# Performance work log

Measured on AMD Instinct MI355X. Metric: run time of the kernel, lower is better.

Reference implementation:

```python
import jax, jax.numpy as jnp
import numpy as np

EPS = 1e-7
KERNELS = ((5, 5), (7, 1), (1, 7))
SCALES = (60, 30, 15, 8)


def avg_pool(x, kh, kw):
    # PyTorch AvgPool2d(kernel, stride=1, padding=(kh//2, kw//2)), count_include_pad=True
    s = jax.lax.reduce_window(x, 0.0, jax.lax.add, (1, 1, kh, kw), (1, 1, 1, 1),
                              ((0, 0), (0, 0), (kh // 2, kh // 2), (kw // 2, kw // 2)))
    return s / (kh * kw)


def resize_bilinear(x, oh, ow):
    # F.interpolate(mode='bilinear', align_corners=True), NCHW
    B, C, H, W = x.shape
    def coords(o, s):
        pos = jnp.arange(o) * ((s - 1) / max(o - 1, 1))
        i0 = jnp.floor(pos).astype(jnp.int32)
        i1 = jnp.minimum(i0 + 1, s - 1)
        w = (pos - i0).astype(x.dtype)
        return w, i0, i1
    wy, y0, y1 = coords(oh, H)
    wx, x0, x1 = coords(ow, W)
    rows = x[:, :, y0, :] * (1 - wy)[None, None, :, None] + x[:, :, y1, :] * wy[None, None, :, None]
    return rows[:, :, :, x0] * (1 - wx) + rows[:, :, :, x1] * wx


def setup_inputs() -> dict:
    key = jax.random.key(0)
    ks = jax.random.split(key, 12)
    B, C, H, shot = 2, 1024, 60, 1
    hid, tdim = 256, 300
    return {
        "weight": jax.random.uniform(ks[0], (B, shot, 1, 1), dtype=jnp.float32),
        "query_feat_4": jax.random.normal(ks[1], (B, C, H, H), dtype=jnp.float32),
        "supp_feats": jax.random.normal(ks[2], (shot, B, C, H, H), dtype=jnp.float32),
        "masks": jax.random.uniform(ks[3], (shot, B, 1, 473, 473), dtype=jnp.float32),
        "k": jax.random.normal(ks[4], (B, hid, H, H), dtype=jnp.float32),
        "text": jax.random.normal(ks[5], (B, tdim), dtype=jnp.float32),
        "prototype": jax.random.normal(ks[6], (B, hid, 1, 1), dtype=jnp.float32),
        "w_q": jax.random.normal(ks[7], (tdim + hid, hid), dtype=jnp.float32) * 0.05,
        "w_k": jax.random.normal(ks[8], (hid, hid), dtype=jnp.float32) * 0.05,
        "w_bl": jax.random.normal(ks[9], (hid, hid), dtype=jnp.float32) * 0.05,
        "w_proj": jax.random.normal(ks[10], (hid, hid), dtype=jnp.float32) * 0.05,
        "b_proj": jnp.zeros((hid,), dtype=jnp.float32),
    }


def reference(weight, query_feat_4, supp_feats, masks, k, text, prototype, w_q, w_k, w_bl, w_proj, b_proj):
    # ---------------- SPM: self-activation prior mask ----------------
    B, C, H, W = query_feat_4.shape
    S = H * W
    # pooled query features per kernel (shared across supports)
    q_pooled = []
    for (kh, kw) in KERNELS:
        tq = avg_pool(query_feat_4, kh, kw).reshape(B, C, S)
        tq_t = jnp.transpose(tq, (0, 2, 1))                    # [B,S,C]
        qn = jnp.sqrt((tq_t ** 2).sum(-1, keepdims=True))      # [B,S,1]
        q_pooled.append((tq_t, qn))

    corr_list = []
    for i in range(supp_feats.shape[0]):  # loop over shot (small, fixed)
        tmp_mask = resize_bilinear(masks[i], H, W)
        s = supp_feats[i] * tmp_mask
        region = []
        for (kh, kw), (tq_t, qn) in zip(KERNELS, q_pooled):
            ts = avg_pool(s, kh, kw).reshape(B, C, S)          # [B,C,S]
            sn = jnp.sqrt((ts ** 2).sum(1, keepdims=True))     # [B,1,S]
            sim = jnp.matmul(tq_t, ts) / (jnp.matmul(qn, sn) + EPS) * qn  # [B,S,S]
            sim = sim.mean(2)                                  # [B,S]
            mn = sim.min(1, keepdims=True)
            mx = sim.max(1, keepdims=True)
            sim = (sim - mn) / (mx - mn + EPS)
            region.append(sim.reshape(B, H, W))
        corr_list.append(jnp.stack(region, 1).mean(1))         # [B,H,W]
    corr = jnp.stack(corr_list, 1)                             # [B,shot,H,W]
    corr1 = (weight * corr).sum(1, keepdims=True)              # [B,1,H,W]
    corr2 = resize_bilinear(corr1, SCALES[1], SCALES[1])
    corr3 = resize_bilinear(corr1, SCALES[2], SCALES[2])
    corr4 = resize_bilinear(corr1, SCALES[3], SCALES[3])

    # ---------------- APA: bi-linear cross-modal attention ----------------
    Bk, hid, h, w = k.shape
    proto = prototype.reshape(Bk, 1, hid)                      # [B,1,hid]
    q = jnp.concatenate([text[:, None, :], proto], axis=-1)    # [B,1,embed]
    kx = jnp.einsum('oi,bihw->bohw', w_k, k).reshape(Bk, hid, h * w)
    kx = jnp.transpose(kx, (0, 2, 1))                          # [B,S,hid]
    qx = jnp.einsum('bqe,eh->bqh', q, w_q)                     # [B,1,hid]
    qw = jnp.einsum('bqh,hd->bqd', qx, w_bl)                   # bi_linear score
    score = jnp.einsum('bqd,bsd->bqs', qw, kx)                 # [B,1,S]
    score = jax.nn.softmax(score, axis=-1)
    out = jnp.einsum('bqs,bsd->bqd', score, kx)
    out = jnp.einsum('bqd,do->bqo', out, w_proj) + b_proj      # proj (dropout=eval no-op)
    out = out + proto
    return corr1, corr2, corr3, corr4, out
```

## Files before the change

### kernel.cpp

```cpp
#include <hip/hip_runtime.h>
#include <math.h>

#define EPSF 1e-7f
#define Bsz 2
#define Cch 1024
#define Hh 60
#define Ssz 3600
#define HID 256
#define TDIM 300
#define MH 473

#define TROWS 15
#define LROWS 21
#define LPITCH 68
#define CPG 8

#define OFF_SN2    0
#define OFF_WMAP   21600
#define OFF_V      43200
#define OFF_U      49344
#define OFF_KBAR   49856
#define OFF_DOTP   50368
#define OFF_SCOREP 395968
#define ZERO_WS    21600
#define ZERO_OUT   9578

__global__ void k_zero(float* __restrict__ ws, float* __restrict__ out) {
    int i = blockIdx.x * 256 + threadIdx.x;
    if (i < ZERO_WS) ws[i] = 0.f;
    else if (i < ZERO_WS + ZERO_OUT) out[i - ZERO_WS] = 0.f;
}

__global__ void __launch_bounds__(256) k_pool_sn2(const float* __restrict__ supp,
                                                  const float* __restrict__ masks,
                                                  float* __restrict__ sn2g) {
    __shared__ float  mk[LROWS * LPITCH];
    __shared__ float2 raw[LROWS * LPITCH];
    __shared__ float2 h5s[LROWS * LPITCH];
    __shared__ float2 h7s[LROWS * LPITCH];
    int tid = threadIdx.x;
    int tile = blockIdx.x;
    int cg = blockIdx.y;
    int b = blockIdx.z;
    int y0 = tile * TROWS;

    const float2 z2 = {0.f, 0.f};
    for (int i = tid; i < LROWS * LPITCH; i += 256) {
        mk[i] = 0.f; raw[i] = z2; h5s[i] = z2; h7s[i] = z2;
    }
    __syncthreads();

    int lr[5], lx[5]; bool lv[5], la[5];
    #pragma unroll
    for (int j = 0; j < 5; ++j) {
        int idx = tid + 256 * j;
        int r = idx / 60, x = idx - 60 * r;
        lr[j] = r; lx[j] = x;
        la[j] = idx < 1260;
        int iy = y0 - 3 + r;
        lv[j] = la[j] && (iy >= 0) && (iy < Hh);
    }
    #pragma unroll
    for (int j = 0; j < 5; ++j)
        if (lv[j]) {
            int iy = y0 - 3 + lr[j];
            mk[lr[j] * LPITCH + 4 + lx[j]] =
                masks[(size_t)b * MH * MH + (size_t)(iy * 8) * MH + lx[j] * 8];
        }

    int orow[4], ox[4]; bool ov[4];
    #pragma unroll
    for (int j = 0; j < 4; ++j) {
        int o = tid + 256 * j;
        int oy = o / 60, x = o - 60 * oy;
        orow[j] = oy + 3; ox[j] = x; ov[j] = o < 900;
    }
    float a0[4] = {0,0,0,0}, a1[4] = {0,0,0,0}, a2[4] = {0,0,0,0};

    const float* chbase = supp + ((size_t)b * Cch + (size_t)cg * CPG) * Ssz + (y0 - 3) * 60;
    float pf0[5], pf1[5];
    #pragma unroll
    for (int j = 0; j < 5; ++j) {
        pf0[j] = lv[j] ? chbase[tid + 256 * j] : 0.f;
        pf1[j] = lv[j] ? chbase[Ssz + tid + 256 * j] : 0.f;
    }

    for (int p = 0; p < CPG / 2; ++p) {
        __syncthreads();
        #pragma unroll
        for (int j = 0; j < 5; ++j)
            if (lv[j]) {
                float m = mk[lr[j] * LPITCH + 4 + lx[j]];
                raw[lr[j] * LPITCH + 4 + lx[j]] = make_float2(pf0[j] * m, pf1[j] * m);
            }
        __syncthreads();
        #pragma unroll
        for (int j = 0; j < 5; ++j)
            if (la[j]) {
                int base = lr[j] * LPITCH + 4 + lx[j];
                float2 m3 = raw[base - 3], m2 = raw[base - 2], m1 = raw[base - 1];
                float2 c0 = raw[base], p1 = raw[base + 1], p2 = raw[base + 2], p3 = raw[base + 3];
                float2 h5, h7;
                h5.x = m2.x + m1.x + c0.x + p1.x + p2.x;
                h5.y = m2.y + m1.y + c0.y + p1.y + p2.y;
                h7.x = h5.x + m3.x + p3.x;
                h7.y = h5.y + m3.y + p3.y;
                h5s[base] = h5; h7s[base] = h7;
            }
        __syncthreads();
        if (p + 1 < CPG / 2) {
            const float* nb = chbase + (size_t)(2 * p + 2) * Ssz;
            #pragma unroll
            for (int j = 0; j < 5; ++j) {
                pf0[j] = lv[j] ? nb[tid + 256 * j] : 0.f;
                pf1[j] = lv[j] ? nb[Ssz + tid + 256 * j] : 0.f;
            }
        }
        #pragma unroll
        for (int j = 0; j < 4; ++j)
            if (ov[j]) {
                int base = orow[j] * LPITCH + 4 + ox[j];
                float2 sa = h5s[base - 2*LPITCH], sb = h5s[base - LPITCH], sc0 = h5s[base];
                float2 sd = h5s[base + LPITCH], se = h5s[base + 2*LPITCH];
                float p55x = (sa.x + sb.x + sc0.x + sd.x + se.x) * (1.f / 25.f);
                float p55y = (sa.y + sb.y + sc0.y + sd.y + se.y) * (1.f / 25.f);
                float2 ra = raw[base - 3*LPITCH], rb = raw[base - 2*LPITCH], rc = raw[base - LPITCH];
                float2 rd = raw[base], re = raw[base + LPITCH], rf = raw[base + 2*LPITCH], rg = raw[base + 3*LPITCH];
                float p71x = (ra.x + rb.x + rc.x + rd.x + re.x + rf.x + rg.x) * (1.f / 7.f);
                float p71y = (ra.y + rb.y + rc.y + rd.y + re.y + rf.y + rg.y) * (1.f / 7.f);
                float2 h7v = h7s[base];
                float p17x = h7v.x * (1.f / 7.f), p17y = h7v.y * (1.f / 7.f);
                a0[j] += p55x * p55x + p55y * p55y;
                a1[j] += p71x * p71x + p71y * p71y;
                a2[j] += p17x * p17x + p17y * p17y;
            }
    }
    float* g0 = sn2g + ((size_t)b * 3 + 0) * Ssz;
    float* g1 = sn2g + ((size_t)b * 3 + 1) * Ssz;
    float* g2 = sn2g + ((size_t)b * 3 + 2) * Ssz;
    #pragma unroll
    for (int j = 0; j < 4; ++j)
        if (ov[j]) {
            int q = (y0 + orow[j] - 3) * 60 + ox[j];
            atomicAdd(&g0[q], a0[j]);
            atomicAdd(&g1[q], a1[j]);
            atomicAdd(&g2[q], a2[j]);
        }
}

__global__ void k_wmap(const float* __restrict__ sn2g, const float* __restrict__ masks,
                       float* __restrict__ wmapg) {
    __shared__ float inv[LROWS * LPITCH];
    int tile = blockIdx.x;
    int bk = blockIdx.y;
    int b = bk / 3, kt = bk % 3;
    int tid = threadIdx.x;
    int y0 = tile * TROWS;
    for (int i = tid; i < LROWS * LPITCH; i += 256) inv[i] = 0.f;
    __syncthreads();
    const float* sn2 = sn2g + (size_t)bk * Ssz;
    #pragma unroll
    for (int j = 0; j < 5; ++j) {
        int idx = tid + 256 * j;
        if (idx < 1260) {
            int r = idx / 60, x = idx - 60 * r;
            int iy = y0 - 3 + r;
            if (iy >= 0 && iy < Hh)
                inv[r * LPITCH + 4 + x] = 1.0f / sqrtf(fmaxf(sn2[iy * 60 + x], 1e-30f));
        }
    }
    __syncthreads();
    int kh = (kt == 0) ? 5 : (kt == 1) ? 7 : 1;
    int kw = (kt == 0) ? 5 : (kt == 2) ? 7 : 1;
    int rh = kh / 2, rw = kw / 2;
    float norm = 1.f / (float)(kh * kw);
    #pragma unroll
    for (int j = 0; j < 4; ++j) {
        int o = tid + 256 * j;
        if (o < 900) {
            int oy = o / 60, x = o - 60 * oy;
            int base = (oy + 3) * LPITCH + 4 + x;
            float s = 0.f;
            for (int dy = -rh; dy <= rh; ++dy)
                for (int dx = -rw; dx <= rw; ++dx)
                    s += inv[base + dy * LPITCH + dx];
            int gy = y0 + oy;
            float m = masks[(size_t)b * MH * MH + (size_t)(gy * 8) * MH + x * 8];
            wmapg[(size_t)bk * Ssz + gy * 60 + x] = s * norm * m;
        }
    }
}

__global__ void k_v(const float* __restrict__ supp, float* __restrict__ ws) {
    int c = blockIdx.x, b = blockIdx.y;
    int tid = threadIdx.x;
    int lane = tid & 63, w = tid >> 6;
    const float4* sp4 = (const float4*)(supp + ((size_t)b * Cch + c) * Ssz);
    const float4* w04 = (const float4*)(ws + OFF_WMAP + (size_t)(b * 3 + 0) * Ssz);
    const float4* w14 = (const float4*)(ws + OFF_WMAP + (size_t)(b * 3 + 1) * Ssz);
    const float4* w24 = (const float4*)(ws + OFF_WMAP + (size_t)(b * 3 + 2) * Ssz);
    float a0 = 0, a1 = 0, a2 = 0;
    #pragma unroll
    for (int j = 0; j < 4; ++j) {
        int idx = tid + 256 * j;
        if (idx < 900) {
            float4 f = sp4[idx];
            float4 g0 = w04[idx], g1 = w14[idx], g2 = w24[idx];
            a0 += f.x * g0.x + f.y * g0.y + f.z * g0.z + f.w * g0.w;
            a1 += f.x * g1.x + f.y * g1.y + f.z * g1.z + f.w * g1.w;
            a2 += f.x * g2.x + f.y * g2.y + f.z * g2.z + f.w * g2.w;
        }
    }
    #pragma unroll
    for (int m = 32; m >= 1; m >>= 1) {
        a0 += __shfl_xor(a0, m, 64);
        a1 += __shfl_xor(a1, m, 64);
        a2 += __shfl_xor(a2, m, 64);
    }
    __shared__ float r[3][4];
    if (lane == 0) { r[0][w] = a0; r[1][w] = a1; r[2][w] = a2; }
    __syncthreads();
    if (tid < 3) {
        float s = r[tid][0] + r[tid][1] + r[tid][2] + r[tid][3];
        ws[OFF_V + (size_t)(b * 3 + tid) * Cch + c] = s;
    }
}

__global__ void k_dot(const float* __restrict__ query, float* __restrict__ ws) {
    int qt = blockIdx.x, cc = blockIdx.y, b = blockIdx.z;
    int q = qt * 256 + threadIdx.x;
    if (q >= Ssz) return;
    const float* v0 = ws + OFF_V + (size_t)(b * 3 + 0) * Cch;
    const float* v1 = ws + OFF_V + (size_t)(b * 3 + 1) * Cch;
    const float* v2 = ws + OFF_V + (size_t)(b * 3 + 2) * Cch;
    float a0 = 0, a1 = 0, a2 = 0;
    int c0 = cc * 64;
    #pragma unroll 8
    for (int c = c0; c < c0 + 64; ++c) {
        float qv = query[((size_t)b * Cch + c) * Ssz + q];
        a0 += qv * v0[c]; a1 += qv * v1[c]; a2 += qv * v2[c];
    }
    float* dst = ws + OFF_DOTP + (size_t)((cc * 2 + b) * 3) * Ssz + q;
    dst[0] = a0; dst[Ssz] = a1; dst[2 * Ssz] = a2;
}

__global__ void __launch_bounds__(1024) k_sim(const float* __restrict__ weight,
                                              float* __restrict__ ws,
                                              float* __restrict__ out) {
    __shared__ float dpad[66 * LPITCH];
    __shared__ float hbuf[66 * LPITCH];
    __shared__ float rmin[16], rmax[16];
    int bk = blockIdx.x; int b = bk / 3; int kt = bk % 3;
    int tid = threadIdx.x;
    int lane = tid & 63, w = tid >> 6;

    const float* dp0 = ws + OFF_DOTP + (size_t)(b * 3 + kt) * Ssz;
    for (int i = tid; i < 66 * LPITCH; i += 1024) {
        int r = i / LPITCH, col = i - r * LPITCH;
        int y = r - 3, x = col - 4;
        float s = 0.f;
        if (y >= 0 && y < Hh && x >= 0 && x < Hh) {
            int q = y * Hh + x;
            #pragma unroll
            for (int g = 0; g < 16; ++g) s += dp0[(size_t)g * 6 * Ssz + q];
        }
        dpad[i] = s;
    }
    __syncthreads();
    if (kt != 1) {
        for (int idx = tid; idx < 66 * 60; idx += 1024) {
            int r = idx / 60, x = idx - 60 * r;
            int base = r * LPITCH + 4 + x;
            if (kt == 0) {
                hbuf[base] = dpad[base - 2] + dpad[base - 1] + dpad[base]
                           + dpad[base + 1] + dpad[base + 2];
            } else {
                hbuf[base] = dpad[base - 3] + dpad[base - 2] + dpad[base - 1] + dpad[base]
                           + dpad[base + 1] + dpad[base + 2] + dpad[base + 3];
            }
        }
    }
    __syncthreads();
    float norm = ((kt == 0) ? (1.f / 25.f) : (1.f / 7.f)) * (1.f / (float)Ssz);
    float vals[4];
    float vmin = INFINITY, vmax = -INFINITY;
    #pragma unroll
    for (int j = 0; j < 4; ++j) {
        int q = tid + j * 1024;
        if (q < Ssz) {
            int y = q / Hh, x = q - y * Hh;
            int base = (y + 3) * LPITCH + 4 + x;
            float s;
            if (kt == 0)
                s = hbuf[base - 2*LPITCH] + hbuf[base - LPITCH] + hbuf[base]
                  + hbuf[base + LPITCH] + hbuf[base + 2*LPITCH];
            else if (kt == 1)
                s = dpad[base - 3*LPITCH] + dpad[base - 2*LPITCH] + dpad[base - LPITCH]
                  + dpad[base] + dpad[base + LPITCH] + dpad[base + 2*LPITCH] + dpad[base + 3*LPITCH];
            else
                s = hbuf[base];
            float val = s * norm;
            vals[j] = val;
            vmin = fminf(vmin, val); vmax = fmaxf(vmax, val);
        }
    }
    #pragma unroll
    for (int m = 32; m >= 1; m >>= 1) {
        vmin = fminf(vmin, __shfl_xor(vmin, m, 64));
        vmax = fmaxf(vmax, __shfl_xor(vmax, m, 64));
    }
    if (lane == 0) { rmin[w] = vmin; rmax[w] = vmax; }
    __syncthreads();
    float mn = rmin[0], mx = rmax[0];
    #pragma unroll
    for (int ww = 1; ww < 16; ++ww) {
        mn = fminf(mn, rmin[ww]); mx = fmaxf(mx, rmax[ww]);
    }
    float inv = 1.f / (mx - mn + EPSF);
    float wq3 = weight[b] * (1.f / 3.f);
    __syncthreads();
    #pragma unroll
    for (int j = 0; j < 4; ++j) {
        int q = tid + j * 1024;
        if (q < Ssz) {
            float vn = (vals[j] - mn) * inv;
            atomicAdd(&out[b * Ssz + q], wq3 * vn);
            hbuf[q] = vn;
        }
    }
    __syncthreads();
    #pragma unroll
    for (int j = 0; j < 2; ++j) {
        int o = tid + j * 1024;
        if (o >= 1189) continue;
        int O, p, outi;
        if (o < 900)       { O = 30; p = o;        outi = 7200 + b * 900 + p; }
        else if (o < 1125) { O = 15; p = o - 900;  outi = 9000 + b * 225 + p; }
        else               { O = 8;  p = o - 1125; outi = 9450 + b * 64 + p; }
        int y = p / O, x = p - y * O;
        float sc = 59.f / (float)(O - 1);
        float py = y * sc, px = x * sc;
        int y0 = (int)floorf(py), x0 = (int)floorf(px);
        int y1 = min(y0 + 1, 59), x1 = min(x0 + 1, 59);
        float wy = py - y0, wx = px - x0;
        float v = hbuf[y0 * 60 + x0] * (1.f - wy) * (1.f - wx)
                + hbuf[y1 * 60 + x0] * wy * (1.f - wx)
                + hbuf[y0 * 60 + x1] * (1.f - wy) * wx
                + hbuf[y1 * 60 + x1] * wy * wx;
        atomicAdd(&out[outi], wq3 * v);
    }
}

__global__ void __launch_bounds__(1024, 1)
k_apa_u(const float* __restrict__ text, const float* __restrict__ proto,
        const float* __restrict__ w_q, const float* __restrict__ w_bl,
        const float* __restrict__ w_k, float* __restrict__ ws) {
    int b = blockIdx.x;
    int tid = threadIdx.x;
    int lane = tid & 63, w = tid >> 6;
    __shared__ float4 p4[16][64];
    __shared__ float qxs[256], qws[256];
    const float4* wq4 = (const float4*)w_q;
    const float4* wbl4 = (const float4*)w_bl;
    const float4* wk4 = (const float4*)w_k;

    float4 acc = {0.f, 0.f, 0.f, 0.f};
    #pragma unroll
    for (int j = 0; j < 35; ++j) {
        int e = w + 16 * j;
        if (e < TDIM + HID) {
            float x = (e < TDIM) ? text[b * TDIM + e] : proto[b * HID + e - TDIM];
            float4 f = wq4[(size_t)e * 64 + lane];
            acc.x += x * f.x; acc.y += x * f.y; acc.z += x * f.z; acc.w += x * f.w;
        }
    }
    p4[w][lane] = acc;
    __syncthreads();
    if (tid < 256) {
        const float* pf = (const float*)p4;
        float s = 0.f;
        #pragma unroll
        for (int ww = 0; ww < 16; ++ww) s += pf[ww * 256 + tid];
        qxs[tid] = s;
    }
    __syncthreads();

    acc.x = acc.y = acc.z = acc.w = 0.f;
    #pragma unroll
    for (int j = 0; j < 16; ++j) {
        int e = w + 16 * j;
        float x = qxs[e];
        float4 f = wbl4[(size_t)e * 64 + lane];
        acc.x += x * f.x; acc.y += x * f.y; acc.z += x * f.z; acc.w += x * f.w;
    }
    p4[w][lane] = acc;
    __syncthreads();
    if (tid < 256) {
        const float* pf = (const float*)p4;
        float s = 0.f;
        #pragma unroll
        for (int ww = 0; ww < 16; ++ww) s += pf[ww * 256 + tid];
        qws[tid] = s;
    }
    __syncthreads();

    acc.x = acc.y = acc.z = acc.w = 0.f;
    #pragma unroll
    for (int j = 0; j < 16; ++j) {
        int e = w + 16 * j;
        float x = qws[e];
        float4 f = wk4[(size_t)e * 64 + lane];
        acc.x += x * f.x; acc.y += x * f.y; acc.z += x * f.z; acc.w += x * f.w;
    }
    p4[w][lane] = acc;
    __syncthreads();
    if (tid < 256) {
        const float* pf = (const float*)p4;
        float s = 0.f;
        #pragma unroll
        for (int ww = 0; ww < 16; ++ww) s += pf[ww * 256 + tid];
        ws[OFF_U + b * HID + tid] = s;
    }
}

__global__ void k_score(const float* __restrict__ kin, float* __restrict__ ws) {
    int st = blockIdx.x, g = blockIdx.y, b = blockIdx.z;
    int s = st * 256 + threadIdx.x;
    if (s >= Ssz) return;
    const float* u = ws + OFF_U + b * HID;
    float acc = 0.f;
    int i0 = g * 64;
    #pragma unroll 8
    for (int i = i0; i < i0 + 64; ++i)
        acc += u[i] * kin[((size_t)b * HID + i) * Ssz + s];
    ws[OFF_SCOREP + (size_t)(g * 2 + b) * Ssz + s] = acc;
}

__global__ void k_kbar(const float* __restrict__ kin, float* __restrict__ ws) {
    int i = blockIdx.x, b = blockIdx.y;
    int tid = threadIdx.x;
    int lane = tid & 63, w = tid >> 6;
    __shared__ float r1[4], r2[4];
    const float4* s0 = (const float4*)(ws + OFF_SCOREP + (size_t)(0 * 2 + b) * Ssz);
    const float4* s1 = (const float4*)(ws + OFF_SCOREP + (size_t)(1 * 2 + b) * Ssz);
    const float4* s2 = (const float4*)(ws + OFF_SCOREP + (size_t)(2 * 2 + b) * Ssz);
    const float4* s3 = (const float4*)(ws + OFF_SCOREP + (size_t)(3 * 2 + b) * Ssz);
    float4 sv[4]; bool act[4];
    float mx = -INFINITY;
    #pragma unroll
    for (int j = 0; j < 4; ++j) {
        int idx = tid + 256 * j;
        act[j] = idx < 900;
        if (act[j]) {
            float4 a = s0[idx], c = s1[idx], d = s2[idx], e = s3[idx];
            float4 v;
            v.x = a.x + c.x + d.x + e.x;
            v.y = a.y + c.y + d.y + e.y;
            v.z = a.z + c.z + d.z + e.z;
            v.w = a.w + c.w + d.w + e.w;
            sv[j] = v;
            mx = fmaxf(mx, fmaxf(fmaxf(v.x, v.y), fmaxf(v.z, v.w)));
        }
    }
    #pragma unroll
    for (int m = 32; m >= 1; m >>= 1) mx = fmaxf(mx, __shfl_xor(mx, m, 64));
    if (lane == 0) r1[w] = mx;
    __syncthreads();
    mx = fmaxf(fmaxf(r1[0], r1[1]), fmaxf(r1[2], r1[3]));
    __syncthreads();
    const float4* kr = (const float4*)(kin + ((size_t)b * HID + i) * Ssz);
    float se = 0.f, wsum = 0.f;
    #pragma unroll
    for (int j = 0; j < 4; ++j) {
        if (act[j]) {
            int idx = tid + 256 * j;
            float4 v = sv[j];
            float ex = expf(v.x - mx), ey = expf(v.y - mx);
            float ez = expf(v.z - mx), ew = expf(v.w - mx);
            se += ex + ey + ez + ew;
            float4 k4 = kr[idx];
            wsum += ex * k4.x + ey * k4.y + ez * k4.z + ew * k4.w;
        }
    }
    #pragma unroll
    for (int m = 32; m >= 1; m >>= 1) {
        se += __shfl_xor(se, m, 64);
        wsum += __shfl_xor(wsum, m, 64);
    }
    if (lane == 0) { r1[w] = se; r2[w] = wsum; }
    __syncthreads();
    if (tid == 0) {
        float seT = r1[0] + r1[1] + r1[2] + r1[3];
        float wsT = r2[0] + r2[1] + r2[2] + r2[3];
        ws[OFF_KBAR + b * HID + i] = wsT / seT;
    }
}

__global__ void __launch_bounds__(1024, 1)
k_apa_out(const float* __restrict__ w_k, const float* __restrict__ w_proj,
          const float* __restrict__ b_proj, const float* __restrict__ proto,
          const float* __restrict__ ws, float* __restrict__ out) {
    int b = blockIdx.x;
    int tid = threadIdx.x;
    int lane = tid & 63, w = tid >> 6;
    __shared__ float4 kbs[64];
    __shared__ float o1s[256];
    __shared__ float4 p4[16][64];
    const float4* wk4 = (const float4*)w_k;
    const float4* wp4 = (const float4*)w_proj;

    if (tid < 64) kbs[tid] = ((const float4*)(ws + OFF_KBAR + b * HID))[tid];
    __syncthreads();

    float4 kb4 = kbs[lane];
    #pragma unroll
    for (int r = 0; r < 16; ++r) {
        int h = w + 16 * r;
        float4 f = wk4[(size_t)h * 64 + lane];
        float p = f.x * kb4.x + f.y * kb4.y + f.z * kb4.z + f.w * kb4.w;
        #pragma unroll
        for (int m = 32; m >= 1; m >>= 1) p += __shfl_xor(p, m, 64);
        if (lane == 0) o1s[h] = p;
    }
    __syncthreads();

    float4 acc = {0.f, 0.f, 0.f, 0.f};
    #pragma unroll
    for (int j = 0; j < 16; ++j) {
        int d = w + 16 * j;
        float x = o1s[d];
        float4 f = wp4[(size_t)d * 64 + lane];
        acc.x += x * f.x; acc.y += x * f.y; acc.z += x * f.z; acc.w += x * f.w;
    }
    p4[w][lane] = acc;
    __syncthreads();
    if (tid < 256) {
        const float* pf = (const float*)p4;
        float s = 0.f;
        #pragma unroll
        for (int ww = 0; ww < 16; ++ww) s += pf[ww * 256 + tid];
        out[9578 + b * HID + tid] = s + b_proj[tid] + proto[b * HID + tid];
    }
}

extern "C" void kernel_launch(void* const* d_in, const int* in_sizes, int n_in,
                              void* d_out, int out_size, void* d_ws, size_t ws_size,
                              hipStream_t stream) {
    const float* weight = (const float*)d_in[0];
    const float* query  = (const float*)d_in[1];
    const float* supp   = (const float*)d_in[2];
    const float* masks  = (const float*)d_in[3];
    const float* kin    = (const float*)d_in[4];
    const float* text   = (const float*)d_in[5];
    const float* proto  = (const float*)d_in[6];
    const float* w_q    = (const float*)d_in[7];
    const float* w_k    = (const float*)d_in[8];
    const float* w_bl   = (const float*)d_in[9];
    const float* w_proj = (const float*)d_in[10];
    const float* b_proj = (const float*)d_in[11];
    float* out = (float*)d_out;
    float* ws  = (float*)d_ws;

    k_zero<<<(ZERO_WS + ZERO_OUT + 255) / 256, 256, 0, stream>>>(ws, out);

    k_pool_sn2<<<dim3(4, Cch / CPG, Bsz), 256, 0, stream>>>(supp, masks, ws + OFF_SN2);
    k_wmap<<<dim3(4, 6), 256, 0, stream>>>(ws + OFF_SN2, masks, ws + OFF_WMAP);
    k_v<<<dim3(Cch, Bsz), 256, 0, stream>>>(supp, ws);
    k_dot<<<dim3(15, 16, Bsz), 256, 0, stream>>>(query, ws);
    k_sim<<<6, 1024, 0, stream>>>(weight, ws, out);

    k_apa_u<<<Bsz, 1024, 0, stream>>>(text, proto, w_q, w_bl, w_k, ws);
    k_score<<<dim3(15, 4, Bsz), 256, 0, stream>>>(kin, ws);
    k_kbar<<<dim3(HID, Bsz), 256, 0, stream>>>(kin, ws);
    k_apa_out<<<Bsz, 1024, 0, stream>>>(w_k, w_proj, b_proj, proto, ws, out);
}
```

Before: 209.5 us.

## Merge kernel chain with in-kernel spin flags, drop atomics and zeroing pass

```diff
diff --git a/kernel.cpp b/kernel.cpp
--- a/kernel.cpp
+++ b/kernel.cpp
@@ -15,25 +15,28 @@
 #define LPITCH 68
 #define CPG 8
 
-#define OFF_SN2    0
-#define OFF_WMAP   21600
-#define OFF_V      43200
-#define OFF_U      49344
-#define OFF_KBAR   49856
-#define OFF_DOTP   50368
-#define OFF_SCOREP 395968
-#define ZERO_WS    21600
-#define ZERO_OUT   9578
-
-__global__ void k_zero(float* __restrict__ ws, float* __restrict__ out) {
-    int i = blockIdx.x * 256 + threadIdx.x;
-    if (i < ZERO_WS) ws[i] = 0.f;
-    else if (i < ZERO_WS + ZERO_OUT) out[i - ZERO_WS] = 0.f;
+#define OFF_PPOOL  0
+#define OFF_WMAP   2764800
+#define OFF_V      2786400
+#define OFF_DOTP   2792544
+#define OFF_NORM   3138144
+#define OFF_SCORE  3159744
+#define OFF_KBAR   3166944
+#define OFF_CNT    3167456
+
+__device__ __forceinline__ void spin_until(int* p, int target) {
+    while (__hip_atomic_load(p, __ATOMIC_ACQUIRE, __HIP_MEMORY_SCOPE_AGENT) < target)
+        __builtin_amdgcn_s_sleep(10);
+}
+__device__ __forceinline__ void publish(int* p, int tid) {
+    __threadfence();
+    __syncthreads();
+    if (tid == 0) __hip_atomic_fetch_add(p, 1, __ATOMIC_RELEASE, __HIP_MEMORY_SCOPE_AGENT);
 }
 
 __global__ void __launch_bounds__(256) k_pool_sn2(const float* __restrict__ supp,
                                                   const float* __restrict__ masks,
-                                                  float* __restrict__ sn2g) {
+                                                  float* __restrict__ ws) {
     __shared__ float  mk[LROWS * LPITCH];
     __shared__ float2 raw[LROWS * LPITCH];
     __shared__ float2 h5s[LROWS * LPITCH];
@@ -135,21 +138,16 @@
                 a2[j] += p17x * p17x + p17y * p17y;
             }
     }
-    float* g0 = sn2g + ((size_t)b * 3 + 0) * Ssz;
-    float* g1 = sn2g + ((size_t)b * 3 + 1) * Ssz;
-    float* g2 = sn2g + ((size_t)b * 3 + 2) * Ssz;
+    float* dst = ws + OFF_PPOOL + (size_t)(cg * 2 + b) * 3 * Ssz;
     #pragma unroll
     for (int j = 0; j < 4; ++j)
         if (ov[j]) {
             int q = (y0 + orow[j] - 3) * 60 + ox[j];
-            atomicAdd(&g0[q], a0[j]);
-            atomicAdd(&g1[q], a1[j]);
-            atomicAdd(&g2[q], a2[j]);
-        }
-}
-
-__global__ void k_wmap(const float* __restrict__ sn2g, const float* __restrict__ masks,
-                       float* __restrict__ wmapg) {
+            dst[q] = a0[j]; dst[Ssz + q] = a1[j]; dst[2 * Ssz + q] = a2[j];
+        }
+}
+
+__global__ void k_wmap(const float* __restrict__ masks, float* __restrict__ ws) {
     __shared__ float inv[LROWS * LPITCH];
     int tile = blockIdx.x;
     int bk = blockIdx.y;
@@ -158,15 +156,20 @@
     int y0 = tile * TROWS;
     for (int i = tid; i < LROWS * LPITCH; i += 256) inv[i] = 0.f;
     __syncthreads();
-    const float* sn2 = sn2g + (size_t)bk * Ssz;
+    const float* pp = ws + OFF_PPOOL + (size_t)(b * 3 + kt) * Ssz;
     #pragma unroll
     for (int j = 0; j < 5; ++j) {
         int idx = tid + 256 * j;
         if (idx < 1260) {
             int r = idx / 60, x = idx - 60 * r;
             int iy = y0 - 3 + r;
-            if (iy >= 0 && iy < Hh)
-                inv[r * LPITCH + 4 + x] = 1.0f / sqrtf(fmaxf(sn2[iy * 60 + x], 1e-30f));
+            if (iy >= 0 && iy < Hh) {
+                int q = iy * 60 + x;
+                float s = 0.f;
+                #pragma unroll 4
+                for (int g = 0; g < 128; ++g) s += pp[(size_t)g * (6 * Ssz) + q];
+                inv[r * LPITCH + 4 + x] = 1.0f / sqrtf(fmaxf(s, 1e-30f));
+            }
         }
     }
     __syncthreads();
@@ -186,180 +189,210 @@
                     s += inv[base + dy * LPITCH + dx];
             int gy = y0 + oy;
             float m = masks[(size_t)b * MH * MH + (size_t)(gy * 8) * MH + x * 8];
-            wmapg[(size_t)bk * Ssz + gy * 60 + x] = s * norm * m;
+            ws[OFF_WMAP + (size_t)bk * Ssz + gy * 60 + x] = s * norm * m;
         }
     }
 }
 
 __global__ void k_v(const float* __restrict__ supp, float* __restrict__ ws) {
-    int c = blockIdx.x, b = blockIdx.y;
-    int tid = threadIdx.x;
-    int lane = tid & 63, w = tid >> 6;
-    const float4* sp4 = (const float4*)(supp + ((size_t)b * Cch + c) * Ssz);
+    int cB = blockIdx.x, b = blockIdx.y;
+    int tid = threadIdx.x, lane = tid & 63, w = tid >> 6;
+    if (cB == 0 && b == 0 && tid < 3) ((int*)(ws + OFF_CNT))[tid] = 0;
+    int c0 = cB * 4;
+    const float4* sp4 = (const float4*)(supp + ((size_t)b * Cch + c0) * Ssz);
     const float4* w04 = (const float4*)(ws + OFF_WMAP + (size_t)(b * 3 + 0) * Ssz);
     const float4* w14 = (const float4*)(ws + OFF_WMAP + (size_t)(b * 3 + 1) * Ssz);
     const float4* w24 = (const float4*)(ws + OFF_WMAP + (size_t)(b * 3 + 2) * Ssz);
-    float a0 = 0, a1 = 0, a2 = 0;
+    float a[4][3];
+    #pragma unroll
+    for (int cc = 0; cc < 4; ++cc) { a[cc][0] = 0; a[cc][1] = 0; a[cc][2] = 0; }
     #pragma unroll
     for (int j = 0; j < 4; ++j) {
         int idx = tid + 256 * j;
         if (idx < 900) {
-            float4 f = sp4[idx];
             float4 g0 = w04[idx], g1 = w14[idx], g2 = w24[idx];
-            a0 += f.x * g0.x + f.y * g0.y + f.z * g0.z + f.w * g0.w;
-            a1 += f.x * g1.x + f.y * g1.y + f.z * g1.z + f.w * g1.w;
-            a2 += f.x * g2.x + f.y * g2.y + f.z * g2.z + f.w * g2.w;
-        }
-    }
-    #pragma unroll
-    for (int m = 32; m >= 1; m >>= 1) {
-        a0 += __shfl_xor(a0, m, 64);
-        a1 += __shfl_xor(a1, m, 64);
-        a2 += __shfl_xor(a2, m, 64);
-    }
-    __shared__ float r[3][4];
-    if (lane == 0) { r[0][w] = a0; r[1][w] = a1; r[2][w] = a2; }
-    __syncthreads();
-    if (tid < 3) {
-        float s = r[tid][0] + r[tid][1] + r[tid][2] + r[tid][3];
-        ws[OFF_V + (size_t)(b * 3 + tid) * Cch + c] = s;
-    }
-}
-
-__global__ void k_dot(const float* __restrict__ query, float* __restrict__ ws) {
-    int qt = blockIdx.x, cc = blockIdx.y, b = blockIdx.z;
-    int q = qt * 256 + threadIdx.x;
-    if (q >= Ssz) return;
-    const float* v0 = ws + OFF_V + (size_t)(b * 3 + 0) * Cch;
-    const float* v1 = ws + OFF_V + (size_t)(b * 3 + 1) * Cch;
-    const float* v2 = ws + OFF_V + (size_t)(b * 3 + 2) * Cch;
-    float a0 = 0, a1 = 0, a2 = 0;
-    int c0 = cc * 64;
-    #pragma unroll 8
-    for (int c = c0; c < c0 + 64; ++c) {
-        float qv = query[((size_t)b * Cch + c) * Ssz + q];
-        a0 += qv * v0[c]; a1 += qv * v1[c]; a2 += qv * v2[c];
-    }
-    float* dst = ws + OFF_DOTP + (size_t)((cc * 2 + b) * 3) * Ssz + q;
-    dst[0] = a0; dst[Ssz] = a1; dst[2 * Ssz] = a2;
-}
-
-__global__ void __launch_bounds__(1024) k_sim(const float* __restrict__ weight,
-                                              float* __restrict__ ws,
-                                              float* __restrict__ out) {
-    __shared__ float dpad[66 * LPITCH];
-    __shared__ float hbuf[66 * LPITCH];
+            #pragma unroll
+            for (int cc = 0; cc < 4; ++cc) {
+                float4 f = sp4[cc * 900 + idx];
+                a[cc][0] += f.x * g0.x + f.y * g0.y + f.z * g0.z + f.w * g0.w;
+                a[cc][1] += f.x * g1.x + f.y * g1.y + f.z * g1.z + f.w * g1.w;
+                a[cc][2] += f.x * g2.x + f.y * g2.y + f.z * g2.z + f.w * g2.w;
+            }
+        }
+    }
+    #pragma unroll
+    for (int m = 32; m >= 1; m >>= 1)
+        #pragma unroll
+        for (int cc = 0; cc < 4; ++cc) {
+            a[cc][0] += __shfl_xor(a[cc][0], m, 64);
+            a[cc][1] += __shfl_xor(a[cc][1], m, 64);
+            a[cc][2] += __shfl_xor(a[cc][2], m, 64);
+        }
+    __shared__ float r[4][3][4];
+    if (lane == 0)
+        #pragma unroll
+        for (int cc = 0; cc < 4; ++cc) {
+            r[cc][0][w] = a[cc][0]; r[cc][1][w] = a[cc][1]; r[cc][2][w] = a[cc][2];
+        }
+    __syncthreads();
+    if (tid < 12) {
+        int cc = tid / 3, kk = tid - cc * 3;
+        float s = r[cc][kk][0] + r[cc][kk][1] + r[cc][kk][2] + r[cc][kk][3];
+        ws[OFF_V + (size_t)(b * 3 + kk) * Cch + c0 + cc] = s;
+    }
+}
+
+__global__ void __launch_bounds__(1024) k_dotsim(const float* __restrict__ query,
+                                                 const float* __restrict__ weight,
+                                                 float* __restrict__ ws,
+                                                 float* __restrict__ out) {
+    __shared__ float sA[66 * LPITCH];
+    __shared__ float sB[66 * LPITCH];
     __shared__ float rmin[16], rmax[16];
-    int bk = blockIdx.x; int b = bk / 3; int kt = bk % 3;
+    int tid = threadIdx.x, bx = blockIdx.x;
+    int lane = tid & 63, w = tid >> 6;
+    int* cnt = (int*)(ws + OFF_CNT);
+
+    if (bx < 128) {
+        int qt = bx & 3, cc = (bx >> 2) & 15, b = bx >> 6;
+        int q = qt * 1024 + tid;
+        if (q < Ssz) {
+            const float* v0 = ws + OFF_V + (size_t)(b * 3 + 0) * Cch;
+            const float* v1 = ws + OFF_V + (size_t)(b * 3 + 1) * Cch;
+            const float* v2 = ws + OFF_V + (size_t)(b * 3 + 2) * Cch;
+            float a0 = 0, a1 = 0, a2 = 0;
+            int c0 = cc * 64;
+            #pragma unroll 8
+            for (int c = c0; c < c0 + 64; ++c) {
+                float qv = query[((size_t)b * Cch + c) * Ssz + q];
+                a0 += qv * v0[c]; a1 += qv * v1[c]; a2 += qv * v2[c];
+            }
+            float* dst = ws + OFF_DOTP + (size_t)((cc * 2 + b) * 3) * Ssz + q;
+            dst[0] = a0; dst[Ssz] = a1; dst[2 * Ssz] = a2;
+        }
+        publish(&cnt[0], tid);
+    } else if (bx < 134) {
+        int bk = bx - 128; int b = bk / 3; int kt = bk % 3;
+        spin_until(&cnt[0], 128);
+        const float* dp0 = ws + OFF_DOTP + (size_t)(b * 3 + kt) * Ssz;
+        for (int i = tid; i < 66 * LPITCH; i += 1024) {
+            int r = i / LPITCH, col = i - r * LPITCH;
+            int y = r - 3, x = col - 4;
+            float s = 0.f;
+            if (y >= 0 && y < Hh && x >= 0 && x < Hh) {
+                int q = y * Hh + x;
+                #pragma unroll
+                for (int g = 0; g < 16; ++g) s += dp0[(size_t)g * 6 * Ssz + q];
+            }
+            sA[i] = s;
+        }
+        __syncthreads();
+        if (kt != 1) {
+            for (int idx = tid; idx < 66 * 60; idx += 1024) {
+                int r = idx / 60, x = idx - 60 * r;
+                int base = r * LPITCH + 4 + x;
+                if (kt == 0)
+                    sB[base] = sA[base - 2] + sA[base - 1] + sA[base] + sA[base + 1] + sA[base + 2];
+                else
+                    sB[base] = sA[base - 3] + sA[base - 2] + sA[base - 1] + sA[base]
+                             + sA[base + 1] + sA[base + 2] + sA[base + 3];
+            }
+        }
+        __syncthreads();
+        float norm = ((kt == 0) ? (1.f / 25.f) : (1.f / 7.f)) * (1.f / (float)Ssz);
+        float vals[4];
+        float vmin = INFINITY, vmax = -INFINITY;
+        #pragma unroll
+        for (int j = 0; j < 4; ++j) {
+            int q = tid + j * 1024;
+            if (q < Ssz) {
+                int y = q / Hh, x = q - y * Hh;
+                int base = (y + 3) * LPITCH + 4 + x;
+                float s;
+                if (kt == 0)
+                    s = sB[base - 2*LPITCH] + sB[base - LPITCH] + sB[base]
+                      + sB[base + LPITCH] + sB[base + 2*LPITCH];
+                else if (kt == 1)
+                    s = sA[base - 3*LPITCH] + sA[base - 2*LPITCH] + sA[base - LPITCH]
+                      + sA[base] + sA[base + LPITCH] + sA[base + 2*LPITCH] + sA[base + 3*LPITCH];
+                else
+                    s = sB[base];
+                float val = s * norm;
+                vals[j] = val;
+                vmin = fminf(vmin, val); vmax = fmaxf(vmax, val);
+            }
+        }
+        #pragma unroll
+        for (int m = 32; m >= 1; m >>= 1) {
+            vmin = fminf(vmin, __shfl_xor(vmin, m, 64));
+            vmax = fmaxf(vmax, __shfl_xor(vmax, m, 64));
+        }
+        if (lane == 0) { rmin[w] = vmin; rmax[w] = vmax; }
+        __syncthreads();
+        float mn = rmin[0], mx = rmax[0];
+        #pragma unroll
+        for (int ww = 1; ww < 16; ++ww) {
+            mn = fminf(mn, rmin[ww]); mx = fmaxf(mx, rmax[ww]);
+        }
+        float inv = 1.f / (mx - mn + EPSF);
+        float* np = ws + OFF_NORM + (size_t)(b * 3 + kt) * Ssz;
+        #pragma unroll
+        for (int j = 0; j < 4; ++j) {
+            int q = tid + j * 1024;
+            if (q < Ssz) np[q] = (vals[j] - mn) * inv;
+        }
+        publish(&cnt[1 + b], tid);
+    } else {
+        int b = bx - 134;
+        spin_until(&cnt[1 + b], 3);
+        float wq3 = weight[b] * (1.f / 3.f);
+        const float* n0 = ws + OFF_NORM + (size_t)(b * 3 + 0) * Ssz;
+        const float* n1 = ws + OFF_NORM + (size_t)(b * 3 + 1) * Ssz;
+        const float* n2 = ws + OFF_NORM + (size_t)(b * 3 + 2) * Ssz;
+        #pragma unroll
+        for (int j = 0; j < 4; ++j) {
+            int q = tid + j * 1024;
+            if (q < Ssz) {
+                float s = n0[q] + n1[q] + n2[q];
+                sA[q] = s;
+                out[b * Ssz + q] = wq3 * s;
+            }
+        }
+        __syncthreads();
+        #pragma unroll
+        for (int j = 0; j < 2; ++j) {
+            int o = tid + j * 1024;
+            if (o >= 1189) continue;
+            int O, p, outi;
+            if (o < 900)       { O = 30; p = o;        outi = 7200 + b * 900 + p; }
+            else if (o < 1125) { O = 15; p = o - 900;  outi = 9000 + b * 225 + p; }
+            else               { O = 8;  p = o - 1125; outi = 9450 + b * 64 + p; }
+            int y = p / O, x = p - y * O;
+            float sc = 59.f / (float)(O - 1);
+            float py = y * sc, px = x * sc;
+            int y0 = (int)floorf(py), x0 = (int)floorf(px);
+            int y1 = min(y0 + 1, 59), x1 = min(x0 + 1, 59);
+            float wy = py - y0, wx = px - x0;
+            float v = sA[y0 * 60 + x0] * (1.f - wy) * (1.f - wx)
+                    + sA[y1 * 60 + x0] * wy * (1.f - wx)
+                    + sA[y0 * 60 + x1] * (1.f - wy) * wx
+                    + sA[y1 * 60 + x1] * wy * wx;
+            out[outi] = wq3 * v;
+        }
+    }
+}
+
+__global__ void __launch_bounds__(1024, 1)
+k_apascore(const float* __restrict__ text, const float* __restrict__ proto,
+           const float* __restrict__ w_q, const float* __restrict__ w_bl,
+           const float* __restrict__ w_k, const float* __restrict__ kin,
+           float* __restrict__ ws) {
+    int st = blockIdx.x, b = blockIdx.y;
     int tid = threadIdx.x;
     int lane = tid & 63, w = tid >> 6;
-
-    const float* dp0 = ws + OFF_DOTP + (size_t)(b * 3 + kt) * Ssz;
-    for (int i = tid; i < 66 * LPITCH; i += 1024) {
-        int r = i / LPITCH, col = i - r * LPITCH;
-        int y = r - 3, x = col - 4;
-        float s = 0.f;
-        if (y >= 0 && y < Hh && x >= 0 && x < Hh) {
-            int q = y * Hh + x;
-            #pragma unroll
-            for (int g = 0; g < 16; ++g) s += dp0[(size_t)g * 6 * Ssz + q];
-        }
-        dpad[i] = s;
-    }
-    __syncthreads();
-    if (kt != 1) {
-        for (int idx = tid; idx < 66 * 60; idx += 1024) {
-            int r = idx / 60, x = idx - 60 * r;
-            int base = r * LPITCH + 4 + x;
-            if (kt == 0) {
-                hbuf[base] = dpad[base - 2] + dpad[base - 1] + dpad[base]
-                           + dpad[base + 1] + dpad[base + 2];
-            } else {
-                hbuf[base] = dpad[base - 3] + dpad[base - 2] + dpad[base - 1] + dpad[base]
-                           + dpad[base + 1] + dpad[base + 2] + dpad[base + 3];
-            }
-        }
-    }
-    __syncthreads();
-    float norm = ((kt == 0) ? (1.f / 25.f) : (1.f / 7.f)) * (1.f / (float)Ssz);
-    float vals[4];
-    float vmin = INFINITY, vmax = -INFINITY;
-    #pragma unroll
-    for (int j = 0; j < 4; ++j) {
-        int q = tid + j * 1024;
-        if (q < Ssz) {
-            int y = q / Hh, x = q - y * Hh;
-            int base = (y + 3) * LPITCH + 4 + x;
-            float s;
-            if (kt == 0)
-                s = hbuf[base - 2*LPITCH] + hbuf[base - LPITCH] + hbuf[base]
-                  + hbuf[base + LPITCH] + hbuf[base + 2*LPITCH];
-            else if (kt == 1)
-                s = dpad[base - 3*LPITCH] + dpad[base - 2*LPITCH] + dpad[base - LPITCH]
-                  + dpad[base] + dpad[base + LPITCH] + dpad[base + 2*LPITCH] + dpad[base + 3*LPITCH];
-            else
-                s = hbuf[base];
-            float val = s * norm;
-            vals[j] = val;
-            vmin = fminf(vmin, val); vmax = fmaxf(vmax, val);
-        }
-    }
-    #pragma unroll
-    for (int m = 32; m >= 1; m >>= 1) {
-        vmin = fminf(vmin, __shfl_xor(vmin, m, 64));
-        vmax = fmaxf(vmax, __shfl_xor(vmax, m, 64));
-    }
-    if (lane == 0) { rmin[w] = vmin; rmax[w] = vmax; }
-    __syncthreads();
-    float mn = rmin[0], mx = rmax[0];
-    #pragma unroll
-    for (int ww = 1; ww < 16; ++ww) {
-        mn = fminf(mn, rmin[ww]); mx = fmaxf(mx, rmax[ww]);
-    }
-    float inv = 1.f / (mx - mn + EPSF);
-    float wq3 = weight[b] * (1.f / 3.f);
-    __syncthreads();
-    #pragma unroll
-    for (int j = 0; j < 4; ++j) {
-        int q = tid + j * 1024;
-        if (q < Ssz) {
-            float vn = (vals[j] - mn) * inv;
-            atomicAdd(&out[b * Ssz + q], wq3 * vn);
-            hbuf[q] = vn;
-        }
-    }
-    __syncthreads();
-    #pragma unroll
-    for (int j = 0; j < 2; ++j) {
-        int o = tid + j * 1024;
-        if (o >= 1189) continue;
-        int O, p, outi;
-        if (o < 900)       { O = 30; p = o;        outi = 7200 + b * 900 + p; }
-        else if (o < 1125) { O = 15; p = o - 900;  outi = 9000 + b * 225 + p; }
-        else               { O = 8;  p = o - 1125; outi = 9450 + b * 64 + p; }
-        int y = p / O, x = p - y * O;
-        float sc = 59.f / (float)(O - 1);
-        float py = y * sc, px = x * sc;
-        int y0 = (int)floorf(py), x0 = (int)floorf(px);
-        int y1 = min(y0 + 1, 59), x1 = min(x0 + 1, 59);
-        float wy = py - y0, wx = px - x0;
-        float v = hbuf[y0 * 60 + x0] * (1.f - wy) * (1.f - wx)
-                + hbuf[y1 * 60 + x0] * wy * (1.f - wx)
-                + hbuf[y0 * 60 + x1] * (1.f - wy) * wx
-                + hbuf[y1 * 60 + x1] * wy * wx;
-        atomicAdd(&out[outi], wq3 * v);
-    }
-}
-
-__global__ void __launch_bounds__(1024, 1)
-k_apa_u(const float* __restrict__ text, const float* __restrict__ proto,
-        const float* __restrict__ w_q, const float* __restrict__ w_bl,
-        const float* __restrict__ w_k, float* __restrict__ ws) {
-    int b = blockIdx.x;
-    int tid = threadIdx.x;
-    int lane = tid & 63, w = tid >> 6;
+    if (st == 0 && b == 0 && tid < 2) ((int*)(ws + OFF_CNT))[4 + tid] = 0;
     __shared__ float4 p4[16][64];
-    __shared__ float qxs[256], qws[256];
+    __shared__ float qxs[256], qws[256], us[256];
     const float4* wq4 = (const float4*)w_q;
     const float4* wbl4 = (const float4*)w_bl;
     const float4* wk4 = (const float4*)w_k;
@@ -419,127 +452,104 @@
         float s = 0.f;
         #pragma unroll
         for (int ww = 0; ww < 16; ++ww) s += pf[ww * 256 + tid];
-        ws[OFF_U + b * HID + tid] = s;
-    }
-}
-
-__global__ void k_score(const float* __restrict__ kin, float* __restrict__ ws) {
-    int st = blockIdx.x, g = blockIdx.y, b = blockIdx.z;
-    int s = st * 256 + threadIdx.x;
-    if (s >= Ssz) return;
-    const float* u = ws + OFF_U + b * HID;
-    float acc = 0.f;
-    int i0 = g * 64;
-    #pragma unroll 8
-    for (int i = i0; i < i0 + 64; ++i)
-        acc += u[i] * kin[((size_t)b * HID + i) * Ssz + s];
-    ws[OFF_SCOREP + (size_t)(g * 2 + b) * Ssz + s] = acc;
-}
-
-__global__ void k_kbar(const float* __restrict__ kin, float* __restrict__ ws) {
-    int i = blockIdx.x, b = blockIdx.y;
-    int tid = threadIdx.x;
+        us[tid] = s;
+    }
+    __syncthreads();
+
+    int sl = tid >> 2, part = tid & 3;
+    if (sl < 240) {
+        int s = st * 240 + sl;
+        const float* kb = kin + ((size_t)b * HID + part * 64) * Ssz + s;
+        const float* up = us + part * 64;
+        float a = 0.f;
+        #pragma unroll 8
+        for (int i = 0; i < 64; ++i) a += up[i] * kb[(size_t)i * Ssz];
+        a += __shfl_xor(a, 1, 64);
+        a += __shfl_xor(a, 2, 64);
+        if (part == 0) ws[OFF_SCORE + (size_t)b * Ssz + s] = a;
+    }
+}
+
+__global__ void __launch_bounds__(256)
+k_kbarout(const float* __restrict__ kin, const float* __restrict__ w_k,
+          const float* __restrict__ w_proj, const float* __restrict__ b_proj,
+          const float* __restrict__ proto, float* __restrict__ ws,
+          float* __restrict__ out) {
+    int bx = blockIdx.x, tid = threadIdx.x;
     int lane = tid & 63, w = tid >> 6;
-    __shared__ float r1[4], r2[4];
-    const float4* s0 = (const float4*)(ws + OFF_SCOREP + (size_t)(0 * 2 + b) * Ssz);
-    const float4* s1 = (const float4*)(ws + OFF_SCOREP + (size_t)(1 * 2 + b) * Ssz);
-    const float4* s2 = (const float4*)(ws + OFF_SCOREP + (size_t)(2 * 2 + b) * Ssz);
-    const float4* s3 = (const float4*)(ws + OFF_SCOREP + (size_t)(3 * 2 + b) * Ssz);
-    float4 sv[4]; bool act[4];
-    float mx = -INFINITY;
-    #pragma unroll
-    for (int j = 0; j < 4; ++j) {
-        int idx = tid + 256 * j;
-        act[j] = idx < 900;
-        if (act[j]) {
-            float4 a = s0[idx], c = s1[idx], d = s2[idx], e = s3[idx];
-            float4 v;
-            v.x = a.x + c.x + d.x + e.x;
-            v.y = a.y + c.y + d.y + e.y;
-            v.z = a.z + c.z + d.z + e.z;
-            v.w = a.w + c.w + d.w + e.w;
-            sv[j] = v;
-            mx = fmaxf(mx, fmaxf(fmaxf(v.x, v.y), fmaxf(v.z, v.w)));
-        }
-    }
-    #pragma unroll
-    for (int m = 32; m >= 1; m >>= 1) mx = fmaxf(mx, __shfl_xor(mx, m, 64));
-    if (lane == 0) r1[w] = mx;
-    __syncthreads();
-    mx = fmaxf(fmaxf(r1[0], r1[1]), fmaxf(r1[2], r1[3]));
-    __syncthreads();
-    const float4* kr = (const float4*)(kin + ((size_t)b * HID + i) * Ssz);
-    float se = 0.f, wsum = 0.f;
-    #pragma unroll
-    for (int j = 0; j < 4; ++j) {
-        if (act[j]) {
+    int* cnt = (int*)(ws + OFF_CNT);
+    if (bx < 512) {
+        int i = bx >> 1, b = bx & 1;
+        __shared__ float r1[4], r2[4];
+        const float4* s4 = (const float4*)(ws + OFF_SCORE + (size_t)b * Ssz);
+        float4 sv[4]; bool act[4];
+        float mx = -INFINITY;
+        #pragma unroll
+        for (int j = 0; j < 4; ++j) {
             int idx = tid + 256 * j;
-            float4 v = sv[j];
-            float ex = expf(v.x - mx), ey = expf(v.y - mx);
-            float ez = expf(v.z - mx), ew = expf(v.w - mx);
-            se += ex + ey + ez + ew;
-            float4 k4 = kr[idx];
-            wsum += ex * k4.x + ey * k4.y + ez * k4.z + ew * k4.w;
-        }
-    }
-    #pragma unroll
-    for (int m = 32; m >= 1; m >>= 1) {
-        se += __shfl_xor(se, m, 64);
-        wsum += __shfl_xor(wsum, m, 64);
-    }
-    if (lane == 0) { r1[w] = se; r2[w] = wsum; }
-    __syncthreads();
-    if (tid == 0) {
-        float seT = r1[0] + r1[1] + r1[2] + r1[3];
-        float wsT = r2[0] + r2[1] + r2[2] + r2[3];
-        ws[OFF_KBAR + b * HID + i] = wsT / seT;
-    }
-}
-
-__global__ void __launch_bounds__(1024, 1)
-k_apa_out(const float* __restrict__ w_k, const float* __restrict__ w_proj,
-          const float* __restrict__ b_proj, const float* __restrict__ proto,
-          const float* __restrict__ ws, float* __restrict__ out) {
-    int b = blockIdx.x;
-    int tid = threadIdx.x;
-    int lane = tid & 63, w = tid >> 6;
-    __shared__ float4 kbs[64];
-    __shared__ float o1s[256];
-    __shared__ float4 p4[16][64];
-    const float4* wk4 = (const float4*)w_k;
-    const float4* wp4 = (const float4*)w_proj;
-
-    if (tid < 64) kbs[tid] = ((const float4*)(ws + OFF_KBAR + b * HID))[tid];
-    __syncthreads();
-
-    float4 kb4 = kbs[lane];
-    #pragma unroll
-    for (int r = 0; r < 16; ++r) {
-        int h = w + 16 * r;
-        float4 f = wk4[(size_t)h * 64 + lane];
-        float p = f.x * kb4.x + f.y * kb4.y + f.z * kb4.z + f.w * kb4.w;
-        #pragma unroll
-        for (int m = 32; m >= 1; m >>= 1) p += __shfl_xor(p, m, 64);
-        if (lane == 0) o1s[h] = p;
-    }
-    __syncthreads();
-
-    float4 acc = {0.f, 0.f, 0.f, 0.f};
-    #pragma unroll
-    for (int j = 0; j < 16; ++j) {
-        int d = w + 16 * j;
-        float x = o1s[d];
-        float4 f = wp4[(size_t)d * 64 + lane];
-        acc.x += x * f.x; acc.y += x * f.y; acc.z += x * f.z; acc.w += x * f.w;
-    }
-    p4[w][lane] = acc;
-    __syncthreads();
-    if (tid < 256) {
-        const float* pf = (const float*)p4;
-        float s = 0.f;
-        #pragma unroll
-        for (int ww = 0; ww < 16; ++ww) s += pf[ww * 256 + tid];
-        out[9578 + b * HID + tid] = s + b_proj[tid] + proto[b * HID + tid];
+            act[j] = idx < 900;
+            if (act[j]) {
+                float4 v = s4[idx];
+                sv[j] = v;
+                mx = fmaxf(mx, fmaxf(fmaxf(v.x, v.y), fmaxf(v.z, v.w)));
+            }
+        }
+        #pragma unroll
+        for (int m = 32; m >= 1; m >>= 1) mx = fmaxf(mx, __shfl_xor(mx, m, 64));
+        if (lane == 0) r1[w] = mx;
+        __syncthreads();
+        mx = fmaxf(fmaxf(r1[0], r1[1]), fmaxf(r1[2], r1[3]));
+        __syncthreads();
+        const float4* kr = (const float4*)(kin + ((size_t)b * HID + i) * Ssz);
+        float se = 0.f, wsum = 0.f;
+        #pragma unroll
+        for (int j = 0; j < 4; ++j) {
+            if (act[j]) {
+                int idx = tid + 256 * j;
+                float4 v = sv[j];
+                float ex = expf(v.x - mx), ey = expf(v.y - mx);
+                float ez = expf(v.z - mx), ew = expf(v.w - mx);
+                se += ex + ey + ez + ew;
+                float4 k4 = kr[idx];
+                wsum += ex * k4.x + ey * k4.y + ez * k4.z + ew * k4.w;
+            }
+        }
+        #pragma unroll
+        for (int m = 32; m >= 1; m >>= 1) {
+            se += __shfl_xor(se, m, 64);
+            wsum += __shfl_xor(wsum, m, 64);
+        }
+        if (lane == 0) { r1[w] = se; r2[w] = wsum; }
+        __syncthreads();
+        if (tid == 0) {
+            float seT = r1[0] + r1[1] + r1[2] + r1[3];
+            float wsT = r2[0] + r2[1] + r2[2] + r2[3];
+            ws[OFF_KBAR + b * HID + i] = wsT / seT;
+        }
+        publish(&cnt[4 + b], tid);
+    } else {
+        int b = bx - 512;
+        spin_until(&cnt[4 + b], 256);
+        __shared__ float4 kbs[64];
+        __shared__ float o1s[256];
+        if (tid < 64) kbs[tid] = ((const float4*)(ws + OFF_KBAR + b * HID))[tid];
+        __syncthreads();
+        const float4* wk4 = (const float4*)w_k;
+        float4 kb4 = kbs[lane];
+        #pragma unroll 8
+        for (int r = 0; r < 64; ++r) {
+            int h = w * 64 + r;
+            float4 f = wk4[(size_t)h * 64 + lane];
+            float p = f.x * kb4.x + f.y * kb4.y + f.z * kb4.z + f.w * kb4.w;
+            #pragma unroll
+            for (int m = 32; m >= 1; m >>= 1) p += __shfl_xor(p, m, 64);
+            if (lane == 0) o1s[h] = p;
+        }
+        __syncthreads();
+        float a2 = b_proj[tid] + proto[b * HID + tid];
+        #pragma unroll 8
+        for (int d = 0; d < 256; ++d) a2 += o1s[d] * w_proj[(size_t)d * HID + tid];
+        out[9578 + b * HID + tid] = a2;
     }
 }
 
@@ -561,16 +571,10 @@
     float* out = (float*)d_out;
     float* ws  = (float*)d_ws;
 
-    k_zero<<<(ZERO_WS + ZERO_OUT + 255) / 256, 256, 0, stream>>>(ws, out);
-
-    k_pool_sn2<<<dim3(4, Cch / CPG, Bsz), 256, 0, stream>>>(supp, masks, ws + OFF_SN2);
-    k_wmap<<<dim3(4, 6), 256, 0, stream>>>(ws + OFF_SN2, masks, ws + OFF_WMAP);
-    k_v<<<dim3(Cch, Bsz), 256, 0, stream>>>(supp, ws);
-    k_dot<<<dim3(15, 16, Bsz), 256, 0, stream>>>(query, ws);
-    k_sim<<<6, 1024, 0, stream>>>(weight, ws, out);
-
-    k_apa_u<<<Bsz, 1024, 0, stream>>>(text, proto, w_q, w_bl, w_k, ws);
-    k_score<<<dim3(15, 4, Bsz), 256, 0, stream>>>(kin, ws);
-    k_kbar<<<dim3(HID, Bsz), 256, 0, stream>>>(kin, ws);
-    k_apa_out<<<Bsz, 1024, 0, stream>>>(w_k, w_proj, b_proj, proto, ws, out);
-}
+    k_pool_sn2<<<dim3(4, 128, 2), 256, 0, stream>>>(supp, masks, ws);
+    k_wmap<<<dim3(4, 6), 256, 0, stream>>>(masks, ws);
+    k_v<<<dim3(256, 2), 256, 0, stream>>>(supp, ws);
+    k_dotsim<<<136, 1024, 0, stream>>>(query, weight, ws, out);
+    k_apascore<<<dim3(15, 2), 1024, 0, stream>>>(text, proto, w_q, w_bl, w_k, kin, ws);
+    k_kbarout<<<514, 256, 0, stream>>>(kin, w_k, w_proj, b_proj, proto, ws, out);
+}
```

Measured after the change: 381.2 us. +81.9%, slower.
